# Performance work log

Measured on AMD Instinct MI355X. Metric: run time of the kernel, lower is better.

## Reference

```python
import jax, jax.numpy as jnp
import numpy as np

N = 50000      # nodes per node type
E = 600000     # edges per edge type
H = 128        # hidden_channels (= in_channels)
OUT = 16       # out_channels
G = 64         # number of graphs in the batch
L = 2          # num_layers
NEG_SLOPE = 0.2


def setup_inputs() -> dict:
    key = jax.random.key(0)
    ks = jax.random.split(key, 13)
    x_paper = jax.random.normal(ks[0], (N, H), jnp.float32)
    x_author = jax.random.normal(ks[1], (N, H), jnp.float32)
    edge_pa = jax.random.randint(ks[2], (2, E), 0, N, jnp.int32)   # paper -> author
    edge_ap = jax.random.randint(ks[3], (2, E), 0, N, jnp.int32)   # author -> paper
    batch_paper = jnp.sort(jax.random.randint(ks[4], (N,), 0, G, jnp.int32))
    batch_author = jnp.sort(jax.random.randint(ks[5], (N,), 0, G, jnp.int32))
    # GAT params, stacked [layer, edge_type, ...]; edge_type 0 = paper->author, 1 = author->paper
    Wsrc = jax.random.normal(ks[6], (L, 2, H, H), jnp.float32) * 0.05
    Wdst = jax.random.normal(ks[7], (L, 2, H, H), jnp.float32) * 0.05
    att_src = jax.random.normal(ks[8], (L, 2, H), jnp.float32) * 0.05
    att_dst = jax.random.normal(ks[9], (L, 2, H), jnp.float32) * 0.05
    bias = jax.random.normal(ks[10], (L, 2, H), jnp.float32) * 0.05
    linW = jax.random.normal(ks[11], (H, OUT), jnp.float32) * 0.05
    linb = jax.random.normal(ks[12], (OUT,), jnp.float32) * 0.05
    return {"x_paper": x_paper, "x_author": x_author, "edge_pa": edge_pa,
            "edge_ap": edge_ap, "batch_paper": batch_paper, "batch_author": batch_author,
            "Wsrc": Wsrc, "Wdst": Wdst, "att_src": att_src, "att_dst": att_dst,
            "bias": bias, "linW": linW, "linb": linb}


def _gat(x_s, x_d, edge, Wsrc, Wdst, a_src_w, a_dst_w, b):
    """Single-head PyG GATConv (bipartite, add_self_loops=False, concat)."""
    src, dst = edge[0], edge[1]
    hs = x_s @ Wsrc                        # [Ns, H]
    hd = x_d @ Wdst                        # [Nd, H]
    a_s = hs @ a_src_w                     # [Ns]
    a_d = hd @ a_dst_w                     # [Nd]
    e = jax.nn.leaky_relu(a_s[src] + a_d[dst], NEG_SLOPE)   # [E]
    nd = x_d.shape[0]
    m = jax.ops.segment_max(e, dst, num_segments=nd)        # segment softmax
    ex = jnp.exp(e - m[dst])
    den = jax.ops.segment_sum(ex, dst, num_segments=nd) + 1e-16
    w = ex / den[dst]                                        # [E]
    out = jax.ops.segment_sum(w[:, None] * hs[src], dst, num_segments=nd)
    return out + b


def reference(x_paper, x_author, edge_pa, edge_ap, batch_paper, batch_author,
              Wsrc, Wdst, att_src, att_dst, bias, linW, linb):
    xp, xa = x_paper, x_author
    for l in range(L):
        out_a = _gat(xp, xa, edge_pa, Wsrc[l, 0], Wdst[l, 0], att_src[l, 0], att_dst[l, 0], bias[l, 0])
        out_p = _gat(xa, xp, edge_ap, Wsrc[l, 1], Wdst[l, 1], att_src[l, 1], att_dst[l, 1], bias[l, 1])
        xp = jax.nn.relu(out_p)
        xa = jax.nn.relu(out_a)
    pooled_p = jax.ops.segment_max(xp, batch_paper, num_segments=G)  # [G, H]
    pooled_a = jax.ops.segment_max(xa, batch_author, num_segments=G)
    return (pooled_p @ linW + linb, pooled_a @ linW + linb)
```

## Files before the change

kernel.cpp:

```cpp
#include <hip/hip_runtime.h>
#include <hip/hip_fp16.h>

constexpr int NN = 50000;
constexpr int NE = 600000;
constexpr int HH = 128;
constexpr int GG = 64;
constexpr int LL = 2;
constexpr int OC = 16;
constexpr float NEG = 0.2f;
constexpr int NBK = (2 * NN + 255) / 256;

typedef _Float16 f16x8 __attribute__((ext_vector_type(8)));
typedef float f32x4 __attribute__((ext_vector_type(4)));

__global__ void k_prevec(const float* __restrict__ Wsrc, const float* __restrict__ Wdst,
                         const float* __restrict__ att_src, const float* __restrict__ att_dst,
                         float* __restrict__ v) {
    int b = blockIdx.x;
    int kind = b >> 2, lt = b & 3;
    const float* W   = (kind ? Wdst : Wsrc) + (size_t)lt * HH * HH;
    const float* att = (kind ? att_dst : att_src) + lt * HH;
    __shared__ float sa[HH];
    int t = threadIdx.x;
    sa[t] = att[t];
    __syncthreads();
    float s = 0.f;
    for (int j = 0; j < HH; ++j) s += W[t * HH + j] * sa[j];
    v[b * HH + t] = s;
}

__global__ void k_wcvt(const float* __restrict__ Wsrc, __half* __restrict__ Wt) {
    int lt = blockIdx.x >> 7;
    int nrow = blockIdx.x & 127;
    int k = threadIdx.x;
    Wt[((size_t)lt * HH + nrow) * HH + k] =
        __float2half_rn(Wsrc[(size_t)lt * HH * HH + (size_t)k * HH + nrow]);
}

__global__ void k_hist2(const int* __restrict__ dpa, const int* __restrict__ dap,
                        int* __restrict__ cnt) {
    int i = blockIdx.x * 256 + threadIdx.x;
    if (i < NE) atomicAdd(&cnt[dpa[i]], 1);
    else if (i < 2 * NE) atomicAdd(&cnt[NN + dap[i - NE]], 1);
}

__global__ void k_scan1(const int* __restrict__ cnt, int* __restrict__ bsum, int n) {
    __shared__ int s[256];
    int i = blockIdx.x * 256 + threadIdx.x;
    s[threadIdx.x] = (i < n) ? cnt[i] : 0;
    __syncthreads();
    for (int off = 128; off > 0; off >>= 1) {
        if (threadIdx.x < off) s[threadIdx.x] += s[threadIdx.x + off];
        __syncthreads();
    }
    if (threadIdx.x == 0) bsum[blockIdx.x] = s[0];
}

__global__ void k_scan2(int* __restrict__ bsum, int nb) {
    __shared__ int s[512];
    int t = threadIdx.x;
    int v = (t < nb) ? bsum[t] : 0;
    s[t] = v;
    __syncthreads();
    for (int off = 1; off < 512; off <<= 1) {
        int x = (t >= off) ? s[t - off] : 0;
        __syncthreads();
        s[t] += x;
        __syncthreads();
    }
    if (t < nb) bsum[t] = s[t] - v;
}

__global__ void k_scan3(const int* __restrict__ cnt, const int* __restrict__ bsum,
                        int* __restrict__ rowptr, int n, int e) {
    __shared__ int s[256];
    int t = threadIdx.x;
    int i = blockIdx.x * 256 + t;
    int v = (i < n) ? cnt[i] : 0;
    s[t] = v;
    __syncthreads();
    for (int off = 1; off < 256; off <<= 1) {
        int x = (t >= off) ? s[t - off] : 0;
        __syncthreads();
        s[t] += x;
        __syncthreads();
    }
    if (i < n) rowptr[i] = bsum[blockIdx.x] + s[t] - v;
    if (i == n - 1) rowptr[n] = e;
}

__global__ void k_binit(const int* __restrict__ rpc, int* __restrict__ bcur) {
    int b = blockIdx.x * 256 + threadIdx.x;
    if (b < NBK) bcur[b] = rpc[b * 256];
}

__global__ __launch_bounds__(256) void k_bucket1(const int* __restrict__ edge_pa,
                                                 const int* __restrict__ edge_ap,
                                                 int* __restrict__ bcur, unsigned* __restrict__ colt) {
    __shared__ int cnt[NBK];
    __shared__ int gpos[NBK];
    int t = threadIdx.x;
    int e0 = blockIdx.x * 4096;
    int m = min(4096, 2 * NE - e0);
    for (int i = t; i < NBK; i += 256) cnt[i] = 0;
    __syncthreads();
    for (int i = t; i < m; i += 256) {
        int e = e0 + i;
        int d = (e < NE) ? edge_pa[NE + e] : NN + edge_ap[NE + (e - NE)];
        atomicAdd(&cnt[d >> 8], 1);
    }
    __syncthreads();
    for (int b = t; b < NBK; b += 256)
        if (cnt[b]) gpos[b] = atomicAdd(&bcur[b], cnt[b]);
    __syncthreads();
    for (int i = t; i < m; i += 256) {
        int e = e0 + i;
        int src, d;
        if (e < NE) { src = edge_pa[e]; d = edge_pa[NE + e]; }
        else        { int j = e - NE; src = edge_ap[j]; d = NN + edge_ap[NE + j]; }
        int p = atomicAdd(&gpos[d >> 8], 1);
        colt[p] = ((unsigned)src << 8) | (unsigned)(d & 255);
    }
}

__global__ __launch_bounds__(256) void k_bucket2(const unsigned* __restrict__ colt,
                                                 const int* __restrict__ rpc, int* __restrict__ colc) {
    __shared__ int cur[257];
    int b = blockIdx.x, t = threadIdx.x;
    int node0 = b * 256;
    int nn2 = min(256, 2 * NN - node0);
    for (int i = t; i <= nn2; i += 256) cur[i] = rpc[node0 + i];
    __syncthreads();
    int g0 = cur[0], g1 = cur[nn2];
    __syncthreads();
    for (int i = g0 + t; i < g1; i += 256) {
        unsigned p = colt[i];
        int pos = atomicAdd(&cur[p & 255], 1);
        colc[pos] = (int)(p >> 8);
    }
}

__global__ __launch_bounds__(256) void k_gemm(const float* __restrict__ X, const __half* __restrict__ Wt,
                                              const float* __restrict__ v1, const float* __restrict__ v2,
                                              __half* __restrict__ Hout,
                                              float* __restrict__ o1, float* __restrict__ o2, int n) {
    int wave = threadIdx.x >> 6;
    int lane = threadIdx.x & 63;
    int r0 = blockIdx.x * 64 + wave * 16;
    int arow = r0 + (lane & 15);
    int kgrp = (lane >> 4) * 8;

    f32x4 acc[8] = {};
    float s1 = 0.f, s2 = 0.f;
#pragma unroll
    for (int ks = 0; ks < 4; ++ks) {
        int k0 = ks * 32 + kgrp;
        float xv[8];
        if (arow < n) {
            float4 x0 = *(const float4*)(X + (size_t)arow * HH + k0);
            float4 x1 = *(const float4*)(X + (size_t)arow * HH + k0 + 4);
            xv[0] = x0.x; xv[1] = x0.y; xv[2] = x0.z; xv[3] = x0.w;
            xv[4] = x1.x; xv[5] = x1.y; xv[6] = x1.z; xv[7] = x1.w;
        } else {
#pragma unroll
            for (int i = 0; i < 8; ++i) xv[i] = 0.f;
        }
        float4 va0 = *(const float4*)(v1 + k0), va1 = *(const float4*)(v1 + k0 + 4);
        float4 vb0 = *(const float4*)(v2 + k0), vb1 = *(const float4*)(v2 + k0 + 4);
        s1 += xv[0] * va0.x + xv[1] * va0.y + xv[2] * va0.z + xv[3] * va0.w
            + xv[4] * va1.x + xv[5] * va1.y + xv[6] * va1.z + xv[7] * va1.w;
        s2 += xv[0] * vb0.x + xv[1] * vb0.y + xv[2] * vb0.z + xv[3] * vb0.w
            + xv[4] * vb1.x + xv[5] * vb1.y + xv[6] * vb1.z + xv[7] * vb1.w;

        f16x8 ahi, alo;
#pragma unroll
        for (int i = 0; i < 8; ++i) {
            _Float16 h = (_Float16)xv[i];
            ahi[i] = h;
            alo[i] = (_Float16)(xv[i] - (float)h);
        }
#pragma unroll
        for (int nt = 0; nt < 8; ++nt) {
            const f16x8 b = *(const f16x8*)(Wt + ((size_t)(nt * 16 + (lane & 15))) * HH + k0);
            acc[nt] = __builtin_amdgcn_mfma_f32_16x16x32_f16(alo, b, acc[nt], 0, 0, 0);
            acc[nt] = __builtin_amdgcn_mfma_f32_16x16x32_f16(ahi, b, acc[nt], 0, 0, 0);
        }
    }

    s1 += __shfl_xor(s1, 16); s1 += __shfl_xor(s1, 32);
    s2 += __shfl_xor(s2, 16); s2 += __shfl_xor(s2, 32);
    if ((lane >> 4) == 0 && arow < n) { o1[arow] = s1; o2[arow] = s2; }

    int srow = r0 + (lane >> 4) * 4;
    int scol = lane & 15;
#pragma unroll
    for (int nt = 0; nt < 8; ++nt) {
#pragma unroll
        for (int reg = 0; reg < 4; ++reg) {
            int gr = srow + reg;
            if (gr < n) Hout[(size_t)gr * HH + nt * 16 + scol] = __float2half_rn(acc[nt][reg]);
        }
    }
}

__global__ __launch_bounds__(256) void k_aggregate2(const int* __restrict__ rpc, const int* __restrict__ colc,
                                                    const __half* __restrict__ H0, const __half* __restrict__ H1,
                                                    const float* __restrict__ as0, const float* __restrict__ ad0,
                                                    const float* __restrict__ as1, const float* __restrict__ ad1,
                                                    const float* __restrict__ bias0, const float* __restrict__ bias1,
                                                    float* __restrict__ XA, float* __restrict__ XP) {
    int w = (blockIdx.x * blockDim.x + threadIdx.x) >> 6;
    int lane = threadIdx.x & 63;
    int type = (w >= NN);
    int node = type ? w - NN : w;
    const __half2* H2  = (const __half2*)(type ? H1 : H0);
    const float* a_s  = type ? as1 : as0;
    float add         = (type ? ad1 : ad0)[node];
    const float* bias = type ? bias1 : bias0;
    float* Xout       = type ? XP : XA;

    int base = rpc[w], end = rpc[w + 1];

    float den = 0.f;
    float2 acc = {0.f, 0.f};

    int j = base;
    for (; j + 8 <= end; j += 8) {
        int s[8]; float c[8]; __half2 h[8];
#pragma unroll
        for (int k = 0; k < 8; ++k) s[k] = colc[j + k];
#pragma unroll
        for (int k = 0; k < 8; ++k) c[k] = a_s[s[k]] + add;
#pragma unroll
        for (int k = 0; k < 8; ++k) h[k] = H2[(size_t)s[k] * (HH / 2) + lane];
#pragma unroll
        for (int k = 0; k < 8; ++k) {
            float cc = c[k];
            cc = cc > 0.f ? cc : NEG * cc;
            float e = __expf(cc);
            den += e;
            float2 f = __half22float2(h[k]);
            acc.x += e * f.x;
            acc.y += e * f.y;
        }
    }
    for (; j + 4 <= end; j += 4) {
        int s[4]; float c[4]; __half2 h[4];
#pragma unroll
        for (int k = 0; k < 4; ++k) s[k] = colc[j + k];
#pragma unroll
        for (int k = 0; k < 4; ++k) c[k] = a_s[s[k]] + add;
#pragma unroll
        for (int k = 0; k < 4; ++k) h[k] = H2[(size_t)s[k] * (HH / 2) + lane];
#pragma unroll
        for (int k = 0; k < 4; ++k) {
            float cc = c[k];
            cc = cc > 0.f ? cc : NEG * cc;
            float e = __expf(cc);
            den += e;
            float2 f = __half22float2(h[k]);
            acc.x += e * f.x;
            acc.y += e * f.y;
        }
    }
    for (; j < end; ++j) {
        int s = colc[j];
        float cc = a_s[s] + add;
        cc = cc > 0.f ? cc : NEG * cc;
        float e = __expf(cc);
        den += e;
        float2 f = __half22float2(H2[(size_t)s * (HH / 2) + lane]);
        acc.x += e * f.x;
        acc.y += e * f.y;
    }

    float inv = 1.f / (den + 1e-16f);
    float2 b = *(const float2*)(bias + lane * 2);
    float2 o;
    o.x = fmaxf(acc.x * inv + b.x, 0.f);
    o.y = fmaxf(acc.y * inv + b.y, 0.f);
    *(float2*)(Xout + (size_t)node * HH + lane * 2) = o;
}

constexpr int POOL_CHUNK = 64;
__global__ __launch_bounds__(256) void k_pool(const float* __restrict__ XPf, const float* __restrict__ XAf,
                                              const int* __restrict__ batch_p, const int* __restrict__ batch_a,
                                              unsigned* __restrict__ pooled, int n, int blocksPerType) {
    int type = blockIdx.x / blocksPerType;
    int blk  = blockIdx.x % blocksPerType;
    const float* X = type ? XAf : XPf;
    const int* batch = type ? batch_a : batch_p;
    unsigned* pool = pooled + type * GG * HH;

    int sub  = threadIdx.x >> 5;
    int lane = threadIdx.x & 31;
    int i0 = blk * POOL_CHUNK + sub * (POOL_CHUNK / 8);
    if (i0 >= n) return;
    int i1 = min(i0 + POOL_CHUNK / 8, n);

    int g = batch[i0];
    float4 m = make_float4(0.f, 0.f, 0.f, 0.f);
    for (int i = i0; i < i1; ++i) {
        int gi = batch[i];
        if (gi != g) {
            unsigned* p = pool + g * HH + lane * 4;
            atomicMax(p + 0, __float_as_uint(m.x));
            atomicMax(p + 1, __float_as_uint(m.y));
            atomicMax(p + 2, __float_as_uint(m.z));
            atomicMax(p + 3, __float_as_uint(m.w));
            m = make_float4(0.f, 0.f, 0.f, 0.f);
            g = gi;
        }
        float4 x = *(const float4*)(X + (size_t)i * HH + lane * 4);
        m.x = fmaxf(m.x, x.x);
        m.y = fmaxf(m.y, x.y);
        m.z = fmaxf(m.z, x.z);
        m.w = fmaxf(m.w, x.w);
    }
    unsigned* p = pool + g * HH + lane * 4;
    atomicMax(p + 0, __float_as_uint(m.x));
    atomicMax(p + 1, __float_as_uint(m.y));
    atomicMax(p + 2, __float_as_uint(m.z));
    atomicMax(p + 3, __float_as_uint(m.w));
}

__global__ void k_final(const unsigned* __restrict__ pooled, const float* __restrict__ linW,
                        const float* __restrict__ linb, float* __restrict__ out) {
    int idx = blockIdx.x * blockDim.x + threadIdx.x;
    if (idx >= 2 * GG * OC) return;
    int p = idx >> 10;
    int g = (idx >> 4) & 63;
    int o = idx & 15;
    const unsigned* row = pooled + (size_t)(p * GG + g) * HH;
    float s = linb[o];
    for (int k = 0; k < HH; ++k) s += __uint_as_float(row[k]) * linW[k * OC + o];
    out[idx] = s;
}

extern "C" void kernel_launch(void* const* d_in, const int* in_sizes, int n_in,
                              void* d_out, int out_size, void* d_ws, size_t ws_size,
                              hipStream_t stream) {
    const float* x_paper  = (const float*)d_in[0];
    const float* x_author = (const float*)d_in[1];
    const int*   edge_pa  = (const int*)d_in[2];
    const int*   edge_ap  = (const int*)d_in[3];
    const int*   batch_p  = (const int*)d_in[4];
    const int*   batch_a  = (const int*)d_in[5];
    const float* Wsrc     = (const float*)d_in[6];
    const float* Wdst     = (const float*)d_in[7];
    const float* att_src  = (const float*)d_in[8];
    const float* att_dst  = (const float*)d_in[9];
    const float* bias     = (const float*)d_in[10];
    const float* linW     = (const float*)d_in[11];
    const float* linb     = (const float*)d_in[12];
    float* out = (float*)d_out;

    size_t off = 0;
    char* base = (char*)d_ws;
    auto alloc = [&](size_t bytes) -> void* {
        void* p = base + off;
        off += (bytes + 255) & ~(size_t)255;
        return p;
    };
    __half* H0 = (__half*)alloc((size_t)NN * HH * 2);
    __half* H1 = (__half*)alloc((size_t)NN * HH * 2);
    float* XP  = (float*)alloc((size_t)NN * HH * 4);
    float* XA  = (float*)alloc((size_t)NN * HH * 4);
    float* as0 = (float*)alloc(NN * 4);
    float* ad0 = (float*)alloc(NN * 4);
    float* as1 = (float*)alloc(NN * 4);
    float* ad1 = (float*)alloc(NN * 4);
    float* vv  = (float*)alloc(8 * HH * 4);
    __half* Wt = (__half*)alloc(4 * HH * HH * 2);
    int* rpc  = (int*)alloc((2 * NN + 1) * 4);
    int* colc = (int*)alloc(2 * NE * 4);
    unsigned* colt = (unsigned*)alloc(2 * NE * 4);
    int* cnt  = (int*)alloc(2 * NN * 4);
    int* bsum = (int*)alloc(2048);
    int* bcur = (int*)alloc(NBK * 4);
    unsigned* pooled = (unsigned*)alloc(2 * GG * HH * 4);

    const int EB2  = (2 * NE + 255) / 256;
    const int NBS2 = (2 * NN + 255) / 256;
    const int CB   = (2 * NE + 4095) / 4096;

    k_prevec<<<8, 128, 0, stream>>>(Wsrc, Wdst, att_src, att_dst, vv);
    k_wcvt<<<512, 128, 0, stream>>>(Wsrc, Wt);

    hipMemsetAsync(cnt, 0, 2 * NN * sizeof(int), stream);
    k_hist2<<<EB2, 256, 0, stream>>>(edge_pa + NE, edge_ap + NE, cnt);
    k_scan1<<<NBS2, 256, 0, stream>>>(cnt, bsum, 2 * NN);
    k_scan2<<<1, 512, 0, stream>>>(bsum, NBS2);
    k_scan3<<<NBS2, 256, 0, stream>>>(cnt, bsum, rpc, 2 * NN, 2 * NE);
    k_binit<<<(NBK + 255) / 256, 256, 0, stream>>>(rpc, bcur);
    k_bucket1<<<CB, 256, 0, stream>>>(edge_pa, edge_ap, bcur, colt);
    k_bucket2<<<NBK, 256, 0, stream>>>(colt, rpc, colc);

    const float* xp = x_paper;
    const float* xa = x_author;
    const int GB = (NN + 63) / 64;
    for (int l = 0; l < LL; ++l) {
        int t0 = l * 2 + 0, t1 = l * 2 + 1;
        k_gemm<<<GB, 256, 0, stream>>>(xp, Wt + (size_t)t0 * HH * HH,
                                       vv + t0 * HH, vv + (4 + t1) * HH, H0, as0, ad1, NN);
        k_gemm<<<GB, 256, 0, stream>>>(xa, Wt + (size_t)t1 * HH * HH,
                                       vv + t1 * HH, vv + (4 + t0) * HH, H1, as1, ad0, NN);
        k_aggregate2<<<25000, 256, 0, stream>>>(rpc, colc, H0, H1, as0, ad0, as1, ad1,
                                                bias + t0 * HH, bias + t1 * HH, XA, XP);
        xp = XP; xa = XA;
    }

    hipMemsetAsync(pooled, 0, 2 * GG * HH * sizeof(unsigned), stream);
    const int PB = (NN + POOL_CHUNK - 1) / POOL_CHUNK;
    k_pool<<<PB * 2, 256, 0, stream>>>(XP, XA, batch_p, batch_a, pooled, NN, PB);
    k_final<<<8, 256, 0, stream>>>(pooled, linW, linb, out);
}
```

Before: 450.8 us.

## Precompute edge attention weights in separate kernel and use half-wave per node aggregation

Edge scores (leaky-relu plus exp of source and destination logits) move out of the aggregation loop into a new per-edge kernel that writes an exp-weight array. Destination indices are stored alongside the sorted CSR so the new kernel can do this. Aggregation now gives each node half a wavefront, loading 4 halves per lane, so one wave serves two nodes. This is meant to improve parallelism and cut the dependent a_s gather inside the aggregation. The cost is an extra kernel launch per layer and extra edge-array traffic (dstc and expw writes and reads).

Result: no change. 456.4 us (+1.2%).

```diff
diff --git a/kernel.cpp b/kernel.cpp
--- a/kernel.cpp
+++ b/kernel.cpp
@@ -124,7 +124,8 @@
 }
 
 __global__ __launch_bounds__(256) void k_bucket2(const unsigned* __restrict__ colt,
-                                                 const int* __restrict__ rpc, int* __restrict__ colc) {
+                                                 const int* __restrict__ rpc,
+                                                 int* __restrict__ colc, int* __restrict__ dstc) {
     __shared__ int cur[257];
     int b = blockIdx.x, t = threadIdx.x;
     int node0 = b * 256;
@@ -137,6 +138,7 @@
         unsigned p = colt[i];
         int pos = atomicAdd(&cur[p & 255], 1);
         colc[pos] = (int)(p >> 8);
+        dstc[pos] = node0 + (int)(p & 255);
     }
 }
 
@@ -203,83 +205,77 @@
     }
 }
 
-__global__ __launch_bounds__(256) void k_aggregate2(const int* __restrict__ rpc, const int* __restrict__ colc,
+__global__ __launch_bounds__(256) void k_score(const int* __restrict__ colc, const int* __restrict__ dstc,
+                                               const float* __restrict__ as0, const float* __restrict__ as1,
+                                               const float* __restrict__ adc, float* __restrict__ expw) {
+    int j = blockIdx.x * 256 + threadIdx.x;
+    if (j >= 2 * NE) return;
+    int src = colc[j];
+    int d   = dstc[j];
+    float c = (j < NE ? as0 : as1)[src] + adc[d];
+    c = c > 0.f ? c : NEG * c;
+    expw[j] = __expf(c);
+}
+
+__global__ __launch_bounds__(256) void k_aggregate3(const int* __restrict__ rpc, const int* __restrict__ colc,
+                                                    const float* __restrict__ expw,
                                                     const __half* __restrict__ H0, const __half* __restrict__ H1,
-                                                    const float* __restrict__ as0, const float* __restrict__ ad0,
-                                                    const float* __restrict__ as1, const float* __restrict__ ad1,
                                                     const float* __restrict__ bias0, const float* __restrict__ bias1,
                                                     float* __restrict__ XA, float* __restrict__ XP) {
-    int w = (blockIdx.x * blockDim.x + threadIdx.x) >> 6;
+    int wid  = (blockIdx.x * blockDim.x + threadIdx.x) >> 6;
     int lane = threadIdx.x & 63;
+    int half = lane >> 5;
+    int sl   = lane & 31;
+    int w = wid * 2 + half;
+    if (w >= 2 * NN) return;
     int type = (w >= NN);
     int node = type ? w - NN : w;
-    const __half2* H2  = (const __half2*)(type ? H1 : H0);
-    const float* a_s  = type ? as1 : as0;
-    float add         = (type ? ad1 : ad0)[node];
+    const __half* Hs  = type ? H1 : H0;
     const float* bias = type ? bias1 : bias0;
     float* Xout       = type ? XP : XA;
 
     int base = rpc[w], end = rpc[w + 1];
 
     float den = 0.f;
-    float2 acc = {0.f, 0.f};
+    float4 acc = {0.f, 0.f, 0.f, 0.f};
 
     int j = base;
-    for (; j + 8 <= end; j += 8) {
-        int s[8]; float c[8]; __half2 h[8];
-#pragma unroll
-        for (int k = 0; k < 8; ++k) s[k] = colc[j + k];
-#pragma unroll
-        for (int k = 0; k < 8; ++k) c[k] = a_s[s[k]] + add;
-#pragma unroll
-        for (int k = 0; k < 8; ++k) h[k] = H2[(size_t)s[k] * (HH / 2) + lane];
-#pragma unroll
-        for (int k = 0; k < 8; ++k) {
-            float cc = c[k];
-            cc = cc > 0.f ? cc : NEG * cc;
-            float e = __expf(cc);
-            den += e;
-            float2 f = __half22float2(h[k]);
-            acc.x += e * f.x;
-            acc.y += e * f.y;
-        }
-    }
     for (; j + 4 <= end; j += 4) {
-        int s[4]; float c[4]; __half2 h[4];
+        int s[4]; float wg[4]; float2 raw[4];
 #pragma unroll
         for (int k = 0; k < 4; ++k) s[k] = colc[j + k];
 #pragma unroll
-        for (int k = 0; k < 4; ++k) c[k] = a_s[s[k]] + add;
-#pragma unroll
-        for (int k = 0; k < 4; ++k) h[k] = H2[(size_t)s[k] * (HH / 2) + lane];
+        for (int k = 0; k < 4; ++k) wg[k] = expw[j + k];
+#pragma unroll
+        for (int k = 0; k < 4; ++k) raw[k] = *(const float2*)(Hs + (size_t)s[k] * HH + sl * 4);
 #pragma unroll
         for (int k = 0; k < 4; ++k) {
-            float cc = c[k];
-            cc = cc > 0.f ? cc : NEG * cc;
-            float e = __expf(cc);
-            den += e;
-            float2 f = __half22float2(h[k]);
-            acc.x += e * f.x;
-            acc.y += e * f.y;
+            den += wg[k];
+            float2 fa = __half22float2(*(const __half2*)&raw[k].x);
+            float2 fb = __half22float2(*(const __half2*)&raw[k].y);
+            acc.x += wg[k] * fa.x; acc.y += wg[k] * fa.y;
+            acc.z += wg[k] * fb.x; acc.w += wg[k] * fb.y;
         }
     }
     for (; j < end; ++j) {
         int s = colc[j];
-        float cc = a_s[s] + add;
-        cc = cc > 0.f ? cc : NEG * cc;
-        float e = __expf(cc);
-        den += e;
-        float2 f = __half22float2(H2[(size_t)s * (HH / 2) + lane]);
-        acc.x += e * f.x;
-        acc.y += e * f.y;
+        float wg = expw[j];
+        float2 raw = *(const float2*)(Hs + (size_t)s * HH + sl * 4);
+        den += wg;
+        float2 fa = __half22float2(*(const __half2*)&raw.x);
+        float2 fb = __half22float2(*(const __half2*)&raw.y);
+        acc.x += wg * fa.x; acc.y += wg * fa.y;
+        acc.z += wg * fb.x; acc.w += wg * fb.y;
     }
 
     float inv = 1.f / (den + 1e-16f);
-    float2 b = *(const float2*)(bias + lane * 2);
-    float2 o;
+    float4 b = *(const float4*)(bias + sl * 4);
+    float4 o;
     o.x = fmaxf(acc.x * inv + b.x, 0.f);
     o.y = fmaxf(acc.y * inv + b.y, 0.f);
-    *(float2*)(Xout + (size_t)node * HH + lane * 2) = o;
+    o.z = fmaxf(acc.z * inv + b.z, 0.f);
+    o.w = fmaxf(acc.w * inv + b.w, 0.f);
+    *(float4*)(Xout + (size_t)node * HH + sl * 4) = o;
 }
 
 constexpr int POOL_CHUNK = 64;
@@ -367,14 +363,15 @@
     float* XP  = (float*)alloc((size_t)NN * HH * 4);
     float* XA  = (float*)alloc((size_t)NN * HH * 4);
     float* as0 = (float*)alloc(NN * 4);
-    float* ad0 = (float*)alloc(NN * 4);
     float* as1 = (float*)alloc(NN * 4);
-    float* ad1 = (float*)alloc(NN * 4);
+    float* adc = (float*)alloc(2 * NN * 4);
     float* vv  = (float*)alloc(8 * HH * 4);
     __half* Wt = (__half*)alloc(4 * HH * HH * 2);
     int* rpc  = (int*)alloc((2 * NN + 1) * 4);
     int* colc = (int*)alloc(2 * NE * 4);
+    int* dstc = (int*)alloc(2 * NE * 4);
     unsigned* colt = (unsigned*)alloc(2 * NE * 4);
+    float* expw = (float*)alloc(2 * NE * 4);
     int* cnt  = (int*)alloc(2 * NN * 4);
     int* bsum = (int*)alloc(2048);
     int* bcur = (int*)alloc(NBK * 4);
@@ -394,7 +391,7 @@
     k_scan3<<<NBS2, 256, 0, stream>>>(cnt, bsum, rpc, 2 * NN, 2 * NE);
     k_binit<<<(NBK + 255) / 256, 256, 0, stream>>>(rpc, bcur);
     k_bucket1<<<CB, 256, 0, stream>>>(edge_pa, edge_ap, bcur, colt);
-    k_bucket2<<<NBK, 256, 0, stream>>>(colt, rpc, colc);
+    k_bucket2<<<NBK, 256, 0, stream>>>(colt, rpc, colc, dstc);
 
     const float* xp = x_paper;
     const float* xa = x_author;
@@ -402,10 +399,11 @@
     for (int l = 0; l < LL; ++l) {
         int t0 = l * 2 + 0, t1 = l * 2 + 1;
         k_gemm<<<GB, 256, 0, stream>>>(xp, Wt + (size_t)t0 * HH * HH,
-                                       vv + t0 * HH, vv + (4 + t1) * HH, H0, as0, ad1, NN);
+                                       vv + t0 * HH, vv + (4 + t1) * HH, H0, as0, adc + NN, NN);
         k_gemm<<<GB, 256, 0, stream>>>(xa, Wt + (size_t)t1 * HH * HH,
-                                       vv + t1 * HH, vv + (4 + t0) * HH, H1, as1, ad0, NN);
-        k_aggregate2<<<25000, 256, 0, stream>>>(rpc, colc, H0, H1, as0, ad0, as1, ad1,
+                                       vv + t1 * HH, vv + (4 + t0) * HH, H1, as1, adc, NN);
+        k_score<<<EB2, 256, 0, stream>>>(colc, dstc, as0, as1, adc, expw);
+        k_aggregate3<<<12500, 256, 0, stream>>>(rpc, colc, expw, H0, H1,
                                                 bias + t0 * HH, bias + t1 * HH, XA, XP);
         xp = XP; xa = XA;
     }
```
